# Kernel optimization log

Hardware: AMD Instinct MI355X
Metric: run time of the kernel (lower is better)

## Reference

```python
import jax, jax.numpy as jnp
import numpy as np

B, T, C, H = 16, 2048, 192, 64

def setup_inputs() -> dict:
    key = jax.random.key(0)
    k1, k2, k3, k4 = jax.random.split(key, 4)
    x = jax.random.normal(k1, (B, T, C), dtype=jnp.float32)
    Wq = jax.random.normal(k2, (C, H), dtype=jnp.float32) * (C ** -0.5)
    Wk = jax.random.normal(k3, (C, H), dtype=jnp.float32) * (C ** -0.5)
    Wv = jax.random.normal(k4, (C, H), dtype=jnp.float32) * (C ** -0.5)
    return {"x": x, "Wq": Wq, "Wk": Wk, "Wv": Wv}

def reference(x, Wq, Wk, Wv):
    # One head of causal self-attention (dropout in eval mode / identity).
    q = x @ Wq                       # [B, T, H]
    k = x @ Wk                       # [B, T, H]
    v = x @ Wv                       # [B, T, H]
    scale = q.shape[-1] ** -0.5
    wei = jnp.einsum('bth,bsh->bts', q, k) * scale   # [B, T, T]
    t = wei.shape[-1]
    causal = jnp.tril(jnp.ones((t, t), dtype=bool))  # tril mask
    wei = jnp.where(causal, wei, -jnp.inf)
    wei = jax.nn.softmax(wei, axis=-1)
    out = jnp.einsum('bts,bsh->bth', wei, v)         # [B, T, H]
    return out
```

## Files before the change

kernel.cpp:

```cpp
#include <hip/hip_runtime.h>

#define B 16
#define T 2048
#define C 192
#define H 64

typedef __bf16 bf16x8 __attribute__((ext_vector_type(8)));
typedef __bf16 bf16x4 __attribute__((ext_vector_type(4)));
typedef float  f32x4  __attribute__((ext_vector_type(4)));

#define MFMA(a, b, c) __builtin_amdgcn_mfma_f32_16x16x32_bf16(a, b, c, 0, 0, 0)

#define SM_BIAS 24.0f

__global__ __launch_bounds__(256) void wtrans_kernel(
    const float* __restrict__ Wq, const float* __restrict__ Wk,
    const float* __restrict__ Wv, __bf16* __restrict__ wt)
{
    const int idx = blockIdx.x * 256 + threadIdx.x;
    const int n = idx / C;
    const int k = idx - n * C;
    const float* W = (n < 64) ? Wq : (n < 128) ? Wk : Wv;
    const int nc = n & 63;
    wt[n * C + k] = (__bf16)W[k * H + nc];
}

__global__ __launch_bounds__(256) void qkv_mfma_kernel(
    const float* __restrict__ x, const __bf16* __restrict__ wt,
    __bf16* __restrict__ qb, __bf16* __restrict__ kb, __bf16* __restrict__ vt)
{
    __shared__ __bf16 Ws[2][192][40];
    __shared__ __bf16 tile[64][72];

    const int tid  = threadIdx.x;
    const int w    = tid >> 6;
    const int lid  = tid & 15;
    const int quad = (tid & 63) >> 4;
    const int m0   = blockIdx.x * 64 + w * 16;

    const float* xrow = x + (size_t)(m0 + lid) * C + quad * 8;
    float4 a0[6], a1[6];
    #pragma unroll
    for (int kc = 0; kc < 6; kc++) {
        a0[kc] = *(const float4*)(xrow + kc * 32);
        a1[kc] = *(const float4*)(xrow + kc * 32 + 4);
    }
    bf16x8 af[6];
    #pragma unroll
    for (int kc = 0; kc < 6; kc++) {
        af[kc][0] = (__bf16)a0[kc].x; af[kc][1] = (__bf16)a0[kc].y;
        af[kc][2] = (__bf16)a0[kc].z; af[kc][3] = (__bf16)a0[kc].w;
        af[kc][4] = (__bf16)a1[kc].x; af[kc][5] = (__bf16)a1[kc].y;
        af[kc][6] = (__bf16)a1[kc].z; af[kc][7] = (__bf16)a1[kc].w;
    }

    bf16x8 wpf[3];
    auto prefW = [&](int kc) {
        #pragma unroll
        for (int i = 0; i < 3; i++) {
            const int p = i * 256 + tid;
            wpf[i] = *(const bf16x8*)(wt + (p >> 2) * C + kc * 32 + (p & 3) * 8);
        }
    };

    f32x4 acc[12] = {};
    prefW(0);
    int cur = 0;
    for (int kc = 0; kc < 6; kc++) {
        #pragma unroll
        for (int i = 0; i < 3; i++) {
            const int p = i * 256 + tid;
            *(bf16x8*)&Ws[cur][p >> 2][(p & 3) * 8] = wpf[i];
        }
        __syncthreads();
        if (kc < 5) prefW(kc + 1);
        #pragma unroll
        for (int nt = 0; nt < 12; nt++) {
            const bf16x8 bfr = *(const bf16x8*)&Ws[cur][nt * 16 + lid][quad * 8];
            acc[nt] = MFMA(af[kc], bfr, acc[nt]);
        }
        cur ^= 1;
    }

    #pragma unroll
    for (int nt = 0; nt < 8; nt++) {
        const int n = nt * 16 + lid;
        __bf16* dst = (n < 64) ? qb : kb;
        const int col = n & 63;
        const float scale = (n < 64) ? 0.1803368801111204f : 1.0f;
        #pragma unroll
        for (int r = 0; r < 4; r++) {
            const int row = m0 + quad * 4 + r;
            dst[(size_t)row * H + col] = (__bf16)(acc[nt][r] * scale);
        }
    }

    #pragma unroll
    for (int nt = 8; nt < 12; nt++) {
        const int col = (nt - 8) * 16 + lid;
        #pragma unroll
        for (int r = 0; r < 4; r++)
            tile[w * 16 + quad * 4 + r][col] = (__bf16)(acc[nt][r]);
    }
    __syncthreads();

    const int bb = blockIdx.x >> 5;
    const int t0 = (blockIdx.x & 31) << 6;
    #pragma unroll
    for (int it = 0; it < 2; ++it) {
        const int h   = it * 32 + (tid >> 3);
        const int tl0 = (tid & 7) * 8;
        bf16x8 d;
        #pragma unroll
        for (int j = 0; j < 8; j++) d[j] = tile[tl0 + j][h];
        *(bf16x8*)(vt + ((size_t)(bb * H + h)) * T + t0 + tl0) = d;
    }
}

__global__ __launch_bounds__(256) void attn_kernel(
    const __bf16* __restrict__ qb,
    const __bf16* __restrict__ kb,
    const __bf16* __restrict__ vt,
    float* __restrict__ out)
{
    __shared__ __bf16 Kb[2][64][72];
    __shared__ __bf16 Vb[2][64][72];

    const int tid  = threadIdx.x;
    const int w    = tid >> 6;
    const int lid  = tid & 15;
    const int quad = (tid & 63) >> 4;

    const int b   = blockIdx.x & 15;
    const int pr  = blockIdx.x >> 4;
    const int qtH = 31 - pr, qtL = pr;
    const int nchH = qtH + 1;
    const int ntot = 33;
    const size_t bbase = (size_t)b * T;

    const int qH = (qtH << 6) + w * 16;
    const int qL = (qtL << 6) + w * 16;

    const __bf16* qrH = qb + (bbase + qH + lid) * H + quad * 8;
    const bf16x8 qfH0 = *(const bf16x8*)(qrH);
    const bf16x8 qfH1 = *(const bf16x8*)(qrH + 32);
    const __bf16* qrL = qb + (bbase + qL + lid) * H + quad * 8;
    const bf16x8 qfL0 = *(const bf16x8*)(qrL);
    const bf16x8 qfL1 = *(const bf16x8*)(qrL + 32);

    const __bf16* kgb = kb + bbase * H;
    const __bf16* vgb = vt + (size_t)b * H * T;

    const int ra = tid >> 3,         ca = (tid & 7) * 8;
    const int rb = (tid + 256) >> 3, cb = (tid & 7) * 8;

    bf16x8 kra, krb, vra, vrb;
    auto prefetch = [&](int key0) {
        kra = *(const bf16x8*)(kgb + (size_t)(key0 + ra) * H + ca);
        krb = *(const bf16x8*)(kgb + (size_t)(key0 + rb) * H + cb);
        vra = *(const bf16x8*)(vgb + (size_t)ra * T + key0 + ca);
        vrb = *(const bf16x8*)(vgb + (size_t)rb * T + key0 + cb);
    };
    auto keyof = [&](int i) { return (i < nchH ? i : i - nchH) << 6; };

    f32x4 O[4] = {};
    float lsum = 0.f;

    auto epilogue = [&](int qw0) {
        float ls = lsum;
        ls += __shfl_xor(ls, 16, 64);
        ls += __shfl_xor(ls, 32, 64);
        #pragma unroll
        for (int ht = 0; ht < 4; ht++)
            #pragma unroll
            for (int r = 0; r < 4; r++) {
                const float Lr = __shfl(ls, quad * 4 + r, 16);
                out[(bbase + qw0 + quad * 4 + r) * H + ht * 16 + lid] =
                    O[ht][r] / Lr;
            }
    };

    bf16x8 cq0 = qfH0, cq1 = qfH1;
    int cqw = qH;

    prefetch(0);
    int cur = 0;
    for (int i = 0; i < ntot; i++) {
        *(bf16x8*)&Kb[cur][ra][ca] = kra;
        *(bf16x8*)&Kb[cur][rb][cb] = krb;
        *(bf16x8*)&Vb[cur][ra][ca] = vra;
        *(bf16x8*)&Vb[cur][rb][cb] = vrb;
        __syncthreads();
        if (i + 1 < ntot) prefetch(keyof(i + 1));

        if (i == nchH) {
            epilogue(cqw);
            #pragma unroll
            for (int ht = 0; ht < 4; ht++) O[ht] = (f32x4){0.f, 0.f, 0.f, 0.f};
            lsum = 0.f;
            cq0 = qfL0; cq1 = qfL1; cqw = qL;
        }

        const int key0 = keyof(i);

        bf16x8 kf[8];
        #pragma unroll
        for (int j = 0; j < 4; j++) {
            kf[2 * j]     = *(const bf16x8*)&Kb[cur][j * 16 + lid][quad * 8];
            kf[2 * j + 1] = *(const bf16x8*)&Kb[cur][j * 16 + lid][32 + quad * 8];
        }

        bf16x8 af0, af1;
        const bool boundary = (key0 + 63 > cqw);
        #pragma unroll
        for (int j = 0; j < 4; j++) {
            f32x4 s = {-SM_BIAS, -SM_BIAS, -SM_BIAS, -SM_BIAS};
            s = MFMA(kf[2 * j], cq0, s);
            s = MFMA(kf[2 * j + 1], cq1, s);
            if (boundary) {
                #pragma unroll
                for (int r = 0; r < 4; r++)
                    if (key0 + j * 16 + quad * 4 + r > cqw + lid) s[r] = -1e30f;
            }
            #pragma unroll
            for (int r = 0; r < 4; r++) {
                const float p = __builtin_amdgcn_exp2f(s[r]);
                lsum += p;
                if      (j == 0) af0[r]     = (__bf16)p;
                else if (j == 1) af0[4 + r] = (__bf16)p;
                else if (j == 2) af1[r]     = (__bf16)p;
                else             af1[4 + r] = (__bf16)p;
            }
        }

        #pragma unroll
        for (int ht = 0; ht < 4; ht++) {
            const __bf16* vr = &Vb[cur][ht * 16 + lid][quad * 4];
            bf16x8 bv0, bv1;
            ((bf16x4*)&bv0)[0] = *(const bf16x4*)(vr);
            ((bf16x4*)&bv0)[1] = *(const bf16x4*)(vr + 16);
            ((bf16x4*)&bv1)[0] = *(const bf16x4*)(vr + 32);
            ((bf16x4*)&bv1)[1] = *(const bf16x4*)(vr + 48);
            O[ht] = MFMA(af0, bv0, O[ht]);
            O[ht] = MFMA(af1, bv1, O[ht]);
        }
        cur ^= 1;
    }
    epilogue(cqw);
}

extern "C" void kernel_launch(void* const* d_in, const int* in_sizes, int n_in,
                              void* d_out, int out_size, void* d_ws, size_t ws_size,
                              hipStream_t stream)
{
    const float* x  = (const float*)d_in[0];
    const float* Wq = (const float*)d_in[1];
    const float* Wk = (const float*)d_in[2];
    const float* Wv = (const float*)d_in[3];

    const size_t BTH = (size_t)B * T * H;
    __bf16* qbuf = (__bf16*)d_ws;
    __bf16* kbuf = qbuf + BTH;
    __bf16* vtb  = kbuf + BTH;
    __bf16* wt   = vtb + BTH;
    float* outp = (float*)d_out;

    wtrans_kernel<<<(C * 3 * H) / 256, 256, 0, stream>>>(Wq, Wk, Wv, wt);
    qkv_mfma_kernel<<<B * T / 64, 256, 0, stream>>>(x, wt, qbuf, kbuf, vtb);
    attn_kernel<<<B * T / 128, 256, 0, stream>>>(qbuf, kbuf, vtb, outp);
}
```

Baseline: 114.0 us.

## Process two key chunks per barrier with quad-buffered K/V shared memory

The attention loop now stages two 64-key chunks of K and V per iteration into a 4-slot shared buffer, so there is one __syncthreads per pair of chunks. Global prefetch of the next pair is issued right after the barrier, and V fragments are loaded from LDS before the QK MFMAs so their latency overlaps with compute. Launch bounds are set to one block per SM to allow more registers for the doubled prefetch buffers. This doubles LDS use and register pressure and may lower occupancy.

```diff
diff --git a/kernel.cpp b/kernel.cpp
--- a/kernel.cpp
+++ b/kernel.cpp
@@ -117,14 +117,14 @@
     }
 }
 
-__global__ __launch_bounds__(256) void attn_kernel(
+__global__ __launch_bounds__(256, 1) void attn_kernel(
     const __bf16* __restrict__ qb,
     const __bf16* __restrict__ kb,
     const __bf16* __restrict__ vt,
     float* __restrict__ out)
 {
-    __shared__ __bf16 Kb[2][64][72];
-    __shared__ __bf16 Vb[2][64][72];
+    __shared__ __bf16 Kb[4][64][72];
+    __shared__ __bf16 Vb[4][64][72];
 
     const int tid  = threadIdx.x;
     const int w    = tid >> 6;
@@ -136,6 +136,7 @@
     const int qtH = 31 - pr, qtL = pr;
     const int nchH = qtH + 1;
     const int ntot = 33;
+    const int nsteps = 17;
     const size_t bbase = (size_t)b * T;
 
     const int qH = (qtH << 6) + w * 16;
@@ -151,17 +152,25 @@
     const __bf16* kgb = kb + bbase * H;
     const __bf16* vgb = vt + (size_t)b * H * T;
 
-    const int ra = tid >> 3,         ca = (tid & 7) * 8;
-    const int rb = (tid + 256) >> 3, cb = (tid & 7) * 8;
-
-    bf16x8 kra, krb, vra, vrb;
-    auto prefetch = [&](int key0) {
-        kra = *(const bf16x8*)(kgb + (size_t)(key0 + ra) * H + ca);
-        krb = *(const bf16x8*)(kgb + (size_t)(key0 + rb) * H + cb);
-        vra = *(const bf16x8*)(vgb + (size_t)ra * T + key0 + ca);
-        vrb = *(const bf16x8*)(vgb + (size_t)rb * T + key0 + cb);
-    };
-    auto keyof = [&](int i) { return (i < nchH ? i : i - nchH) << 6; };
+    const int ra = tid >> 3, ca = (tid & 7) * 8;
+    const int rb = ra + 32,  cb = ca;
+
+    auto keyof = [&](int i) {
+        if (i >= ntot) i = ntot - 1;
+        return (i < nchH ? i : i - nchH) << 6;
+    };
+
+    bf16x8 kra[2], krb[2], vra[2], vrb[2];
+    auto prefetch2 = [&](int s) {
+        #pragma unroll
+        for (int u = 0; u < 2; u++) {
+            const int key0 = keyof(2 * s + u);
+            kra[u] = *(const bf16x8*)(kgb + (size_t)(key0 + ra) * H + ca);
+            krb[u] = *(const bf16x8*)(kgb + (size_t)(key0 + rb) * H + cb);
+            vra[u] = *(const bf16x8*)(vgb + (size_t)ra * T + key0 + ca);
+            vrb[u] = *(const bf16x8*)(vgb + (size_t)rb * T + key0 + cb);
+        }
+    };
 
     f32x4 O[4] = {};
     float lsum = 0.f;
@@ -183,66 +192,79 @@
     bf16x8 cq0 = qfH0, cq1 = qfH1;
     int cqw = qH;
 
-    prefetch(0);
+    prefetch2(0);
     int cur = 0;
-    for (int i = 0; i < ntot; i++) {
-        *(bf16x8*)&Kb[cur][ra][ca] = kra;
-        *(bf16x8*)&Kb[cur][rb][cb] = krb;
-        *(bf16x8*)&Vb[cur][ra][ca] = vra;
-        *(bf16x8*)&Vb[cur][rb][cb] = vrb;
+    for (int s = 0; s < nsteps; s++) {
+        #pragma unroll
+        for (int u = 0; u < 2; u++) {
+            const int buf = 2 * cur + u;
+            *(bf16x8*)&Kb[buf][ra][ca] = kra[u];
+            *(bf16x8*)&Kb[buf][rb][cb] = krb[u];
+            *(bf16x8*)&Vb[buf][ra][ca] = vra[u];
+            *(bf16x8*)&Vb[buf][rb][cb] = vrb[u];
+        }
         __syncthreads();
-        if (i + 1 < ntot) prefetch(keyof(i + 1));
-
-        if (i == nchH) {
-            epilogue(cqw);
-            #pragma unroll
-            for (int ht = 0; ht < 4; ht++) O[ht] = (f32x4){0.f, 0.f, 0.f, 0.f};
-            lsum = 0.f;
-            cq0 = qfL0; cq1 = qfL1; cqw = qL;
-        }
-
-        const int key0 = keyof(i);
-
-        bf16x8 kf[8];
-        #pragma unroll
-        for (int j = 0; j < 4; j++) {
-            kf[2 * j]     = *(const bf16x8*)&Kb[cur][j * 16 + lid][quad * 8];
-            kf[2 * j + 1] = *(const bf16x8*)&Kb[cur][j * 16 + lid][32 + quad * 8];
-        }
-
-        bf16x8 af0, af1;
-        const bool boundary = (key0 + 63 > cqw);
-        #pragma unroll
-        for (int j = 0; j < 4; j++) {
-            f32x4 s = {-SM_BIAS, -SM_BIAS, -SM_BIAS, -SM_BIAS};
-            s = MFMA(kf[2 * j], cq0, s);
-            s = MFMA(kf[2 * j + 1], cq1, s);
-            if (boundary) {
+        if (s + 1 < nsteps) prefetch2(s + 1);
+
+        #pragma unroll
+        for (int u = 0; u < 2; u++) {
+            const int i = 2 * s + u;
+            if (i >= ntot) break;
+            if (i == nchH) {
+                epilogue(cqw);
                 #pragma unroll
-                for (int r = 0; r < 4; r++)
-                    if (key0 + j * 16 + quad * 4 + r > cqw + lid) s[r] = -1e30f;
-            }
-            #pragma unroll
-            for (int r = 0; r < 4; r++) {
-                const float p = __builtin_amdgcn_exp2f(s[r]);
-                lsum += p;
-                if      (j == 0) af0[r]     = (__bf16)p;
-                else if (j == 1) af0[4 + r] = (__bf16)p;
-                else if (j == 2) af1[r]     = (__bf16)p;
-                else             af1[4 + r] = (__bf16)p;
-            }
-        }
-
-        #pragma unroll
-        for (int ht = 0; ht < 4; ht++) {
-            const __bf16* vr = &Vb[cur][ht * 16 + lid][quad * 4];
-            bf16x8 bv0, bv1;
-            ((bf16x4*)&bv0)[0] = *(const bf16x4*)(vr);
-            ((bf16x4*)&bv0)[1] = *(const bf16x4*)(vr + 16);
-            ((bf16x4*)&bv1)[0] = *(const bf16x4*)(vr + 32);
-            ((bf16x4*)&bv1)[1] = *(const bf16x4*)(vr + 48);
-            O[ht] = MFMA(af0, bv0, O[ht]);
-            O[ht] = MFMA(af1, bv1, O[ht]);
+                for (int ht = 0; ht < 4; ht++) O[ht] = (f32x4){0.f,0.f,0.f,0.f};
+                lsum = 0.f;
+                cq0 = qfL0; cq1 = qfL1; cqw = qL;
+            }
+            const int key0 = keyof(i);
+            const int buf  = 2 * cur + u;
+
+            bf16x8 kf[8];
+            #pragma unroll
+            for (int j = 0; j < 4; j++) {
+                kf[2*j]   = *(const bf16x8*)&Kb[buf][j * 16 + lid][quad * 8];
+                kf[2*j+1] = *(const bf16x8*)&Kb[buf][j * 16 + lid][32 + quad * 8];
+            }
+            bf16x8 bv0[4], bv1[4];
+            #pragma unroll
+            for (int ht = 0; ht < 4; ht++) {
+                const __bf16* vr = &Vb[buf][ht * 16 + lid][quad * 4];
+                ((bf16x4*)&bv0[ht])[0] = *(const bf16x4*)(vr);
+                ((bf16x4*)&bv0[ht])[1] = *(const bf16x4*)(vr + 16);
+                ((bf16x4*)&bv1[ht])[0] = *(const bf16x4*)(vr + 32);
+                ((bf16x4*)&bv1[ht])[1] = *(const bf16x4*)(vr + 48);
+            }
+
+            bf16x8 af0, af1;
+            const bool boundary = (key0 + 63 > cqw);
+            #pragma unroll
+            for (int j = 0; j < 4; j++) {
+                f32x4 sS = {-SM_BIAS, -SM_BIAS, -SM_BIAS, -SM_BIAS};
+                sS = MFMA(kf[2*j], cq0, sS);
+                sS = MFMA(kf[2*j+1], cq1, sS);
+                if (boundary) {
+                    #pragma unroll
+                    for (int r = 0; r < 4; r++)
+                        if (key0 + j * 16 + quad * 4 + r > cqw + lid)
+                            sS[r] = -1e30f;
+                }
+                #pragma unroll
+                for (int r = 0; r < 4; r++) {
+                    const float p = __builtin_amdgcn_exp2f(sS[r]);
+                    lsum += p;
+                    if      (j == 0) af0[r]     = (__bf16)p;
+                    else if (j == 1) af0[4 + r] = (__bf16)p;
+                    else if (j == 2) af1[r]     = (__bf16)p;
+                    else             af1[4 + r] = (__bf16)p;
+                }
+            }
+
+            #pragma unroll
+            for (int ht = 0; ht < 4; ht++) {
+                O[ht] = MFMA(af0, bv0[ht], O[ht]);
+                O[ht] = MFMA(af1, bv1[ht], O[ht]);
+            }
         }
         cur ^= 1;
     }
```

After: 114.6 us. About the same (+0.5%).
